# Performance work log

Measured on AMD Instinct MI355X. Metric: run time of the kernel, lower is better.

Reference implementation:

```python
import jax, jax.numpy as jnp
import numpy as np

V, E, H = 32000, 128, 256
B, S, T = 32, 128, 128


def lstm(emb, Wih, Whh, bih, bhh, h0, c0):
    """Single-layer batch_first LSTM matching torch.nn.LSTM (gate order i,f,g,o).
    emb: [B,T,E] -> (outputs [B,T,H], h_T [B,H], c_T [B,H])."""
    b = bih + bhh  # [4H]
    xg = jnp.einsum('bte,ge->btg', emb, Wih) + b  # precompute input gates [B,T,4H]

    def step(carry, xg_t):
        h, c = carry
        gates = xg_t + h @ Whh.T  # [B,4H]
        i, f, g, o = jnp.split(gates, 4, axis=-1)
        i, f, o = jax.nn.sigmoid(i), jax.nn.sigmoid(f), jax.nn.sigmoid(o)
        g = jnp.tanh(g)
        c = f * c + i * g
        h = o * jnp.tanh(c)
        return (h, c), h

    (hT, cT), hs = jax.lax.scan(step, (h0, c0), jnp.swapaxes(xg, 0, 1))
    return jnp.swapaxes(hs, 0, 1), hT, cT


def setup_inputs() -> dict:
    key = jax.random.key(0)
    ks = jax.random.split(key, 14)
    s_e, s_h = 1.0 / np.sqrt(H), 1.0 / np.sqrt(H)
    return {
        'x': jax.random.randint(ks[0], (B, S), 0, V),
        'y': jax.random.randint(ks[1], (B, T), 0, V),
        'enc_emb': jax.random.normal(ks[2], (V, E), jnp.float32),
        'dec_emb': jax.random.normal(ks[3], (V, E), jnp.float32),
        'Wih_enc': jax.random.uniform(ks[4], (4 * H, E), jnp.float32, -s_e, s_e),
        'Whh_enc': jax.random.uniform(ks[5], (4 * H, H), jnp.float32, -s_h, s_h),
        'bih_enc': jax.random.uniform(ks[6], (4 * H,), jnp.float32, -s_h, s_h),
        'bhh_enc': jax.random.uniform(ks[7], (4 * H,), jnp.float32, -s_h, s_h),
        'Wih_dec': jax.random.uniform(ks[8], (4 * H, E), jnp.float32, -s_e, s_e),
        'Whh_dec': jax.random.uniform(ks[9], (4 * H, H), jnp.float32, -s_h, s_h),
        'bih_dec': jax.random.uniform(ks[10], (4 * H,), jnp.float32, -s_h, s_h),
        'bhh_dec': jax.random.uniform(ks[11], (4 * H,), jnp.float32, -s_h, s_h),
        'W_out': jax.random.uniform(ks[12], (V, H), jnp.float32, -s_h, s_h),
        'b_out': jax.random.uniform(ks[13], (V,), jnp.float32, -s_h, s_h),
    }


def reference(x, y, enc_emb, dec_emb, Wih_enc, Whh_enc, bih_enc, bhh_enc,
              Wih_dec, Whh_dec, bih_dec, bhh_dec, W_out, b_out):
    h0 = jnp.zeros((x.shape[0], H), jnp.float32)
    c0 = jnp.zeros((x.shape[0], H), jnp.float32)
    # encoder
    x_emb = enc_emb[x]  # [B,S,E]
    _, h, c = lstm(x_emb, Wih_enc, Whh_enc, bih_enc, bhh_enc, h0, c0)
    # decoder (teacher forcing)
    y_emb = dec_emb[y]  # [B,T,E]
    dec_out, _, _ = lstm(y_emb, Wih_dec, Whh_dec, bih_dec, bhh_dec, h, c)
    logits = jnp.einsum('bth,vh->btv', dec_out, W_out) + b_out  # [B,T,V]
    return logits
```

## Files before the change

kernel.cpp:

```cpp
#include <hip/hip_runtime.h>


typedef _Float16 half2v __attribute__((ext_vector_type(2)));
typedef short bf16x8 __attribute__((ext_vector_type(8)));
typedef float f32x4 __attribute__((ext_vector_type(4)));

__device__ __forceinline__ unsigned short f2h_bits(float f) {
  _Float16 h = (_Float16)f;
  return __builtin_bit_cast(unsigned short, h);
}

__device__ __forceinline__ unsigned short f2bf_bits(float f) {
  unsigned u = __builtin_bit_cast(unsigned, f);
  u += 0x7fffu + ((u >> 16) & 1u);
  return (unsigned short)(u >> 16);
}

__device__ __forceinline__ float fdot2u(unsigned wu, unsigned hu, float acc) {
#if defined(__has_builtin) && __has_builtin(__builtin_amdgcn_fdot2)
  return __builtin_amdgcn_fdot2(__builtin_bit_cast(half2v, wu),
                                __builtin_bit_cast(half2v, hu), acc, false);
#else
  half2v a = __builtin_bit_cast(half2v, wu);
  half2v b = __builtin_bit_cast(half2v, hu);
  return acc + (float)a[0] * (float)b[0] + (float)a[1] * (float)b[1];
#endif
}

__device__ __forceinline__ float tanh_fast(float x) {
  float e = __expf(2.f * x);
  return 1.f - 2.f / (e + 1.f);
}

__device__ __forceinline__ float sigmoid_fast(float x) {
  return 1.f / (1.f + __expf(-x));
}

__device__ __forceinline__ void gload_lds16(const void* g, void* l) {
#if defined(__has_builtin) && __has_builtin(__builtin_amdgcn_global_load_lds)
  __builtin_amdgcn_global_load_lds(
      (const __attribute__((address_space(1))) void*)g,
      (__attribute__((address_space(3))) void*)l, 16, 0, 0);
#else
  *(uint4*)l = *(const uint4*)g;
#endif
}

__global__ void prep_kernel(const float* __restrict__ WhhE, const float* __restrict__ WhhD,
                            const float* __restrict__ Wout,
                            unsigned* __restrict__ WhhP, unsigned short* __restrict__ WoutB) {
  int i = blockIdx.x * blockDim.x + threadIdx.x;
  int stride = gridDim.x * blockDim.x;
  for (int idx = i; idx < 262144; idx += stride) {
    int p = idx >> 17;
    int rem = idx & 131071;
    int d = rem >> 10;
    int g = rem & 1023;
    const float* W = p ? WhhD : WhhE;
    float a = W[g * 256 + 2 * d];
    float b = W[g * 256 + 2 * d + 1];
    WhhP[idx] = (unsigned)f2h_bits(a) | ((unsigned)f2h_bits(b) << 16);
  }
  for (int idx = i; idx < 8192000; idx += stride) {
    WoutB[idx] = f2bf_bits(Wout[idx]);
  }
}

__global__ __launch_bounds__(256, 2) void xg_kernel(
    const int* __restrict__ x, const int* __restrict__ y,
    const float* __restrict__ enc_emb, const float* __restrict__ dec_emb,
    const float* __restrict__ Wih_enc, const float* __restrict__ Wih_dec,
    float* __restrict__ xg) {
  __shared__ float Al[64][132];
  __shared__ float Bl[64][132];
  __shared__ int tok[64];
  const int nb = blockIdx.x;
  const int mbb = blockIdx.y;
  const int m0 = mbb * 64;
  const int p = mbb >> 6;
  const int tid = threadIdx.x;

  if (tid < 64) {
    int mloc = (m0 + tid) & 4095;
    tok[tid] = p ? y[mloc] : x[mloc];
  }
  __syncthreads();

  const float* emb = p ? dec_emb : enc_emb;
  const float* Wih = p ? Wih_dec : Wih_enc;
  {
    int ri = tid & 63, seg = tid >> 6;
    const float* er = emb + (size_t)tok[ri] * 128 + seg * 32;
    const float* wr = Wih + (size_t)(nb * 64 + ri) * 128 + seg * 32;
#pragma unroll
    for (int c = 0; c < 8; ++c) {
      *(float4*)&Al[ri][seg * 32 + c * 4] = *(const float4*)&er[c * 4];
      *(float4*)&Bl[ri][seg * 32 + c * 4] = *(const float4*)&wr[c * 4];
    }
  }
  __syncthreads();

  const int tx = tid & 15, ty = tid >> 4;
  float acc[4][4];
#pragma unroll
  for (int mm = 0; mm < 4; ++mm)
#pragma unroll
    for (int nn = 0; nn < 4; ++nn) acc[mm][nn] = 0.f;

  for (int k4 = 0; k4 < 32; ++k4) {
    float4 av[4], bv[4];
#pragma unroll
    for (int mm = 0; mm < 4; ++mm) av[mm] = *(const float4*)&Al[mm * 16 + ty][k4 * 4];
#pragma unroll
    for (int nn = 0; nn < 4; ++nn) bv[nn] = *(const float4*)&Bl[nn * 16 + tx][k4 * 4];
#pragma unroll
    for (int mm = 0; mm < 4; ++mm)
#pragma unroll
      for (int nn = 0; nn < 4; ++nn) {
        acc[mm][nn] = fmaf(av[mm].x, bv[nn].x, acc[mm][nn]);
        acc[mm][nn] = fmaf(av[mm].y, bv[nn].y, acc[mm][nn]);
        acc[mm][nn] = fmaf(av[mm].z, bv[nn].z, acc[mm][nn]);
        acc[mm][nn] = fmaf(av[mm].w, bv[nn].w, acc[mm][nn]);
      }
  }
#pragma unroll
  for (int mm = 0; mm < 4; ++mm)
#pragma unroll
    for (int nn = 0; nn < 4; ++nn)
      xg[(size_t)(m0 + mm * 16 + ty) * 1024 + nb * 64 + nn * 16 + tx] = acc[mm][nn];
}

__global__ __launch_bounds__(512, 2) void lstm_kernel(
    const float* __restrict__ xg, const unsigned* __restrict__ WhhP,
    const float* __restrict__ bih_enc, const float* __restrict__ bhh_enc,
    const float* __restrict__ bih_dec, const float* __restrict__ bhh_dec,
    unsigned short* __restrict__ decO,
    unsigned* __restrict__ xbuf,
    unsigned* __restrict__ xflag) {
  const int w = blockIdx.x;
  const int b = w & 31;
  const int r = w >> 5;
  const int t = threadIdx.x;
  const int q = t >> 7;
  const int jj = t & 127;
  const int j = r * 128 + jj;
  const int g = q * 256 + j;

  __shared__ __align__(16) unsigned h2[128];
  __shared__ float gact[4][128];

  if (t < 128) h2[t] = 0u;
  float c_r = 0.f;
  __syncthreads();

  unsigned wqd[128];
  float bias_g = 0.f;

  for (int s = 0; s < 256; ++s) {
    const int p = s >> 7;
    const int tt = s & 127;

    if ((s & 127) == 0) {
      const unsigned* base = WhhP + (p << 17);
#pragma unroll
      for (int d = 0; d < 128; ++d) {
        int dsrc = (d + (r << 6)) & 127;
        wqd[d] = base[(dsrc << 10) + g];
      }
      bias_g = p ? (bih_dec[g] + bhh_dec[g]) : (bih_enc[g] + bhh_enc[g]);
    }

    const float xgv = xg[(size_t)(((p << 5) + b) * 128 + tt) * 1024 + g];

    float a0 = 0.f, a1 = 0.f, a2 = 0.f, a3 = 0.f;
#pragma unroll
    for (int c = 0; c < 16; ++c) {
      const uint4 hv = *(const uint4*)&h2[(((r << 4) | c) << 2)];
      a0 = fdot2u(wqd[4 * c + 0], hv.x, a0);
      a1 = fdot2u(wqd[4 * c + 1], hv.y, a1);
      a2 = fdot2u(wqd[4 * c + 2], hv.z, a2);
      a3 = fdot2u(wqd[4 * c + 3], hv.w, a3);
    }

    if (s > 0 && t < 64) {
      const int pw = w ^ 32;
      const int slot = ((s - 1) << 6) + pw;
      while (__hip_atomic_load(&xflag[slot], __ATOMIC_ACQUIRE,
                               __HIP_MEMORY_SCOPE_AGENT) != (unsigned)s) {
      }
      h2[((1 ^ r) << 6) + t] = xbuf[(size_t)slot * 64 + t];
    }
    __syncthreads();

#pragma unroll
    for (int c = 0; c < 16; ++c) {
      const uint4 hv = *(const uint4*)&h2[((((1 ^ r) << 4) | c) << 2)];
      a0 = fdot2u(wqd[64 + 4 * c + 0], hv.x, a0);
      a1 = fdot2u(wqd[64 + 4 * c + 1], hv.y, a1);
      a2 = fdot2u(wqd[64 + 4 * c + 2], hv.z, a2);
      a3 = fdot2u(wqd[64 + 4 * c + 3], hv.w, a3);
    }
    const float accf = bias_g + xgv + ((a0 + a1) + (a2 + a3));

    const float act = (q == 2) ? tanh_fast(accf) : sigmoid_fast(accf);
    gact[q][jj] = act;
    __syncthreads();

    if (q == 0) {
      const float iv = gact[0][jj];
      const float fv = gact[1][jj];
      const float gv = gact[2][jj];
      const float ov = gact[3][jj];
      c_r = fv * c_r + iv * gv;
      const float hh = ov * tanh_fast(c_r);
      ((unsigned short*)h2)[j] = f2h_bits(hh);
      if (p) decO[(size_t)((b << 7) + tt) * 256 + j] = f2bf_bits(hh);
      const float hn = __shfl_down(hh, 1, 64);
      if (!(jj & 1)) {
        const unsigned dw = (unsigned)f2h_bits(hh) | ((unsigned)f2h_bits(hn) << 16);
        __hip_atomic_store(&xbuf[(size_t)((s << 6) + w) * 64 + (jj >> 1)], dw,
                           __ATOMIC_RELAXED, __HIP_MEMORY_SCOPE_AGENT);
      }
    }
    __syncthreads();
    if (t == 0)
      __hip_atomic_store(&xflag[(s << 6) + w], (unsigned)(s + 1), __ATOMIC_RELEASE,
                         __HIP_MEMORY_SCOPE_AGENT);
  }
}

__global__ __launch_bounds__(256, 2) void proj_kernel(
    const unsigned short* __restrict__ A,
    const unsigned short* __restrict__ Bw,
    const float* __restrict__ bias, float* __restrict__ out) {
  __shared__ unsigned short Al[128 * 128];
  __shared__ unsigned short Bl[128 * 128];
  const int mb = blockIdx.x;
  const int nb = blockIdx.y;
  const int tid = threadIdx.x;
  const int wv = tid >> 6, ln = tid & 63;
  const int wm = wv & 1, wn = wv >> 1;
  const int l16 = ln & 15, lq = ln >> 4;

  f32x4 acc[4][4] = {};

  for (int kc = 0; kc < 2; ++kc) {
#pragma unroll
    for (int it = 0; it < 8; ++it) {
      int st = it * 256 + tid;
      int m = st >> 4, k8 = st & 15;
      const unsigned short* gp =
          A + (size_t)(mb * 128 + m) * 256 + kc * 128 + ((k8 ^ (m & 15)) << 3);
      gload_lds16(gp, &Al[st << 3]);
    }
#pragma unroll
    for (int it = 0; it < 8; ++it) {
      int st = it * 256 + tid;
      int m = st >> 4, k8 = st & 15;
      const unsigned short* gp =
          Bw + (size_t)(nb * 128 + m) * 256 + kc * 128 + ((k8 ^ (m & 15)) << 3);
      gload_lds16(gp, &Bl[st << 3]);
    }
    asm volatile("s_waitcnt vmcnt(0)" ::: "memory");
    __syncthreads();

#pragma unroll
    for (int ks = 0; ks < 4; ++ks) {
      const int k8 = (ks << 2) + lq;
      bf16x8 af[4], bf[4];
#pragma unroll
      for (int mt = 0; mt < 4; ++mt) {
        int m = (wm << 6) + (mt << 4) + l16;
        af[mt] = *(const bf16x8*)&Al[(m << 7) + ((k8 ^ (m & 15)) << 3)];
      }
#pragma unroll
      for (int nt = 0; nt < 4; ++nt) {
        int n = (wn << 6) + (nt << 4) + l16;
        bf[nt] = *(const bf16x8*)&Bl[(n << 7) + ((k8 ^ (n & 15)) << 3)];
      }
#pragma unroll
      for (int mt = 0; mt < 4; ++mt)
#pragma unroll
        for (int nt = 0; nt < 4; ++nt)
          acc[mt][nt] = __builtin_amdgcn_mfma_f32_16x16x32_bf16(af[mt], bf[nt],
                                                                acc[mt][nt], 0, 0, 0);
    }
    __syncthreads();
  }

#pragma unroll
  for (int nt = 0; nt < 4; ++nt) {
    const int gcol = nb * 128 + (wn << 6) + (nt << 4) + l16;
    const float bs = bias[gcol];
#pragma unroll
    for (int mt = 0; mt < 4; ++mt) {
      const int grow0 = mb * 128 + (wm << 6) + (mt << 4) + (lq << 2);
#pragma unroll
      for (int rr = 0; rr < 4; ++rr)
        out[(size_t)(grow0 + rr) * 32000 + gcol] = acc[mt][nt][rr] + bs;
    }
  }
}

extern "C" void kernel_launch(void* const* d_in, const int* in_sizes, int n_in,
                              void* d_out, int out_size, void* d_ws, size_t ws_size,
                              hipStream_t stream) {
  const int* x = (const int*)d_in[0];
  const int* y = (const int*)d_in[1];
  const float* enc_emb = (const float*)d_in[2];
  const float* dec_emb = (const float*)d_in[3];
  const float* Wih_enc = (const float*)d_in[4];
  const float* Whh_enc = (const float*)d_in[5];
  const float* bih_enc = (const float*)d_in[6];
  const float* bhh_enc = (const float*)d_in[7];
  const float* Wih_dec = (const float*)d_in[8];
  const float* Whh_dec = (const float*)d_in[9];
  const float* bih_dec = (const float*)d_in[10];
  const float* bhh_dec = (const float*)d_in[11];
  const float* W_out = (const float*)d_in[12];
  const float* b_out = (const float*)d_in[13];

  char* ws = (char*)d_ws;
  float* xg = (float*)ws;
  unsigned* WhhP = (unsigned*)(ws + 33554432);
  unsigned short* WoutB = (unsigned short*)(ws + 34603008);
  unsigned short* decO = (unsigned short*)(ws + 50987008);
  unsigned* xbuf = (unsigned*)(ws + 53084160);
  unsigned* xflag = (unsigned*)(ws + 57278464);
  if (ws_size < 57344000) return;

  prep_kernel<<<4096, 256, 0, stream>>>(Whh_enc, Whh_dec, W_out, WhhP, WoutB);
  xg_kernel<<<dim3(16, 128), 256, 0, stream>>>(x, y, enc_emb, dec_emb, Wih_enc, Wih_dec, xg);
  lstm_kernel<<<64, 512, 0, stream>>>(xg, WhhP, bih_enc, bhh_enc, bih_dec, bhh_dec,
                                      decO, xbuf, xflag);
  proj_kernel<<<dim3(32, 250), 256, 0, stream>>>(decO, WoutB, b_out, (float*)d_out);
}
```

Before: 1.468 ms.

## Run each batch's LSTM in one 1024-thread block, dropping cross-block flag exchange

The recurrent kernel now uses one 1024-thread workgroup per batch row instead of two 512-thread workgroups that swapped half of h through global memory with atomic flags every step. Each thread holds 92 packed weight pairs in registers and reads the remaining 36 from a 144KB LDS array. The next step's xg value is prefetched one step ahead. This removes the per-step global-memory handshake and spin-wait, at the cost of half as many workgroups, heavy register pressure at 1024 threads, and LDS reads for part of the weights.

Measured after the change: 1.278 ms. 12.9% less time.

```diff
diff --git a/kernel.cpp b/kernel.cpp
--- a/kernel.cpp
+++ b/kernel.cpp
@@ -130,31 +130,29 @@
       xg[(size_t)(m0 + mm * 16 + ty) * 1024 + nb * 64 + nn * 16 + tx] = acc[mm][nn];
 }
 
-__global__ __launch_bounds__(512, 2) void lstm_kernel(
+__global__ __launch_bounds__(1024, 1) void lstm_kernel(
     const float* __restrict__ xg, const unsigned* __restrict__ WhhP,
     const float* __restrict__ bih_enc, const float* __restrict__ bhh_enc,
     const float* __restrict__ bih_dec, const float* __restrict__ bhh_dec,
-    unsigned short* __restrict__ decO,
-    unsigned* __restrict__ xbuf,
-    unsigned* __restrict__ xflag) {
-  const int w = blockIdx.x;
-  const int b = w & 31;
-  const int r = w >> 5;
+    unsigned short* __restrict__ decO) {
+  const int b = blockIdx.x;
   const int t = threadIdx.x;
-  const int q = t >> 7;
-  const int jj = t & 127;
-  const int j = r * 128 + jj;
-  const int g = q * 256 + j;
+  const int g = t;
+  const int q = t >> 8;
+  const int j = t & 255;
 
   __shared__ __align__(16) unsigned h2[128];
-  __shared__ float gact[4][128];
+  __shared__ float gact[4][256];
+  __shared__ unsigned WL[18 * 2048];
 
   if (t < 128) h2[t] = 0u;
   float c_r = 0.f;
   __syncthreads();
 
-  unsigned wqd[128];
+  unsigned wqd[92];
   float bias_g = 0.f;
+
+  float xgv_n = xg[(size_t)(b << 7) * 1024 + g];
 
   for (int s = 0; s < 256; ++s) {
     const int p = s >> 7;
@@ -163,69 +161,58 @@
     if ((s & 127) == 0) {
       const unsigned* base = WhhP + (p << 17);
 #pragma unroll
-      for (int d = 0; d < 128; ++d) {
-        int dsrc = (d + (r << 6)) & 127;
-        wqd[d] = base[(dsrc << 10) + g];
-      }
+      for (int d = 0; d < 92; ++d) wqd[d] = base[(d << 10) + g];
+#pragma unroll
+      for (int dd = 0; dd < 36; ++dd)
+        WL[((dd >> 1) << 11) + (g << 1) + (dd & 1)] = base[((92 + dd) << 10) + g];
       bias_g = p ? (bih_dec[g] + bhh_dec[g]) : (bih_enc[g] + bhh_enc[g]);
     }
 
-    const float xgv = xg[(size_t)(((p << 5) + b) * 128 + tt) * 1024 + g];
+    const float xgv = xgv_n;
+    if (s < 255) {
+      const int sn = s + 1;
+      xgv_n = xg[(size_t)(((sn >> 7) << 12) + (b << 7) + (sn & 127)) * 1024 + g];
+    }
 
     float a0 = 0.f, a1 = 0.f, a2 = 0.f, a3 = 0.f;
 #pragma unroll
-    for (int c = 0; c < 16; ++c) {
-      const uint4 hv = *(const uint4*)&h2[(((r << 4) | c) << 2)];
+    for (int c = 0; c < 23; ++c) {
+      const uint4 hv = *(const uint4*)&h2[c << 2];
       a0 = fdot2u(wqd[4 * c + 0], hv.x, a0);
       a1 = fdot2u(wqd[4 * c + 1], hv.y, a1);
       a2 = fdot2u(wqd[4 * c + 2], hv.z, a2);
       a3 = fdot2u(wqd[4 * c + 3], hv.w, a3);
     }
-
-    if (s > 0 && t < 64) {
-      const int pw = w ^ 32;
-      const int slot = ((s - 1) << 6) + pw;
-      while (__hip_atomic_load(&xflag[slot], __ATOMIC_ACQUIRE,
-                               __HIP_MEMORY_SCOPE_AGENT) != (unsigned)s) {
-      }
-      h2[((1 ^ r) << 6) + t] = xbuf[(size_t)slot * 64 + t];
-    }
+#pragma unroll
+    for (int c = 23; c < 32; ++c) {
+      const uint4 hv = *(const uint4*)&h2[c << 2];
+      const int dp0 = (4 * c - 92) >> 1;
+      const uint2 w01 = *(const uint2*)&WL[(dp0 << 11) + (g << 1)];
+      const uint2 w23 = *(const uint2*)&WL[((dp0 + 1) << 11) + (g << 1)];
+      a0 = fdot2u(w01.x, hv.x, a0);
+      a1 = fdot2u(w01.y, hv.y, a1);
+      a2 = fdot2u(w23.x, hv.z, a2);
+      a3 = fdot2u(w23.y, hv.w, a3);
+    }
+    const float accf = bias_g + xgv + ((a0 + a1) + (a2 + a3));
+
+    const float act = (q == 2) ? tanh_fast(accf) : sigmoid_fast(accf);
+    gact[q][j] = act;
     __syncthreads();
 
-#pragma unroll
-    for (int c = 0; c < 16; ++c) {
-      const uint4 hv = *(const uint4*)&h2[((((1 ^ r) << 4) | c) << 2)];
-      a0 = fdot2u(wqd[64 + 4 * c + 0], hv.x, a0);
-      a1 = fdot2u(wqd[64 + 4 * c + 1], hv.y, a1);
-      a2 = fdot2u(wqd[64 + 4 * c + 2], hv.z, a2);
-      a3 = fdot2u(wqd[64 + 4 * c + 3], hv.w, a3);
-    }
-    const float accf = bias_g + xgv + ((a0 + a1) + (a2 + a3));
-
-    const float act = (q == 2) ? tanh_fast(accf) : sigmoid_fast(accf);
-    gact[q][jj] = act;
-    __syncthreads();
-
-    if (q == 0) {
-      const float iv = gact[0][jj];
-      const float fv = gact[1][jj];
-      const float gv = gact[2][jj];
-      const float ov = gact[3][jj];
+    if (t < 256) {
+      const float iv = gact[0][t];
+      const float fv = gact[1][t];
+      const float gv = gact[2][t];
+      const float ov = gact[3][t];
       c_r = fv * c_r + iv * gv;
       const float hh = ov * tanh_fast(c_r);
-      ((unsigned short*)h2)[j] = f2h_bits(hh);
-      if (p) decO[(size_t)((b << 7) + tt) * 256 + j] = f2bf_bits(hh);
+      if (p) decO[(size_t)((b << 7) + tt) * 256 + t] = f2bf_bits(hh);
       const float hn = __shfl_down(hh, 1, 64);
-      if (!(jj & 1)) {
-        const unsigned dw = (unsigned)f2h_bits(hh) | ((unsigned)f2h_bits(hn) << 16);
-        __hip_atomic_store(&xbuf[(size_t)((s << 6) + w) * 64 + (jj >> 1)], dw,
-                           __ATOMIC_RELAXED, __HIP_MEMORY_SCOPE_AGENT);
-      }
+      if (!(t & 1))
+        h2[t >> 1] = (unsigned)f2h_bits(hh) | ((unsigned)f2h_bits(hn) << 16);
     }
     __syncthreads();
-    if (t == 0)
-      __hip_atomic_store(&xflag[(s << 6) + w], (unsigned)(s + 1), __ATOMIC_RELEASE,
-                         __HIP_MEMORY_SCOPE_AGENT);
   }
 }
 
@@ -325,13 +312,10 @@
   unsigned* WhhP = (unsigned*)(ws + 33554432);
   unsigned short* WoutB = (unsigned short*)(ws + 34603008);
   unsigned short* decO = (unsigned short*)(ws + 50987008);
-  unsigned* xbuf = (unsigned*)(ws + 53084160);
-  unsigned* xflag = (unsigned*)(ws + 57278464);
   if (ws_size < 57344000) return;
 
   prep_kernel<<<4096, 256, 0, stream>>>(Whh_enc, Whh_dec, W_out, WhhP, WoutB);
   xg_kernel<<<dim3(16, 128), 256, 0, stream>>>(x, y, enc_emb, dec_emb, Wih_enc, Wih_dec, xg);
-  lstm_kernel<<<64, 512, 0, stream>>>(xg, WhhP, bih_enc, bhh_enc, bih_dec, bhh_dec,
-                                      decO, xbuf, xflag);
+  lstm_kernel<<<32, 1024, 0, stream>>>(xg, WhhP, bih_enc, bhh_enc, bih_dec, bhh_dec, decO);
   proj_kernel<<<dim3(32, 250), 256, 0, stream>>>(decO, WoutB, b_out, (float*)d_out);
 }
```
